# Performance work log

Measured on AMD Instinct MI355X. Metric: run time of the kernel, lower is better.

The kernel has to match this reference:

```python
import math
import jax, jax.numpy as jnp
import numpy as np

DIM = 4096
N_HEADS = 32
N_KV_HEADS = 8
HEAD_DIM = DIM // N_HEADS  # 128
N_REP = N_HEADS // N_KV_HEADS  # 4
BSZ = 2
SEQLEN = 2048
ROPE_THETA = 500000.0


def setup_inputs() -> dict:
    key = jax.random.key(0)
    ks = jax.random.split(key, 6)
    s = 0.02
    x = jax.random.normal(ks[0], (BSZ, SEQLEN, DIM), dtype=jnp.float32)
    wq = jax.random.normal(ks[1], (DIM, N_HEADS * HEAD_DIM), dtype=jnp.float32) * s
    wk = jax.random.normal(ks[2], (DIM, N_KV_HEADS * HEAD_DIM), dtype=jnp.float32) * s
    wv = jax.random.normal(ks[3], (DIM, N_KV_HEADS * HEAD_DIM), dtype=jnp.float32) * s
    wo = jax.random.normal(ks[4], (N_HEADS * HEAD_DIM, DIM), dtype=jnp.float32) * s
    # RoPE frequencies (real cos/sin form of complex freqs_cis)
    inv_freq = 1.0 / (ROPE_THETA ** (jnp.arange(0, HEAD_DIM, 2, dtype=jnp.float32) / HEAD_DIM))
    t = jnp.arange(SEQLEN, dtype=jnp.float32)
    angles = jnp.outer(t, inv_freq)  # [S, HEAD_DIM/2]
    freqs_cos = jnp.cos(angles)
    freqs_sin = jnp.sin(angles)
    # additive causal mask [S, S]: 0 on/below diag, -1e9 above
    mask = jnp.where(jnp.tril(jnp.ones((SEQLEN, SEQLEN), dtype=bool)), 0.0, -1e9).astype(jnp.float32)
    return {"x": x, "wq": wq, "wk": wk, "wv": wv, "wo": wo,
            "freqs_cos": freqs_cos, "freqs_sin": freqs_sin, "mask": mask,
            "start_pos": 0}


def _apply_rope(t, cos, sin):
    # t: [B, S, H, HD]; cos/sin: [S, HD/2] -> broadcast [1, S, 1, HD/2]
    b, s, h, hd = t.shape
    tr = t.reshape(b, s, h, hd // 2, 2)
    te, to = tr[..., 0], tr[..., 1]
    c = cos[None, :, None, :]
    sn = sin[None, :, None, :]
    oe = te * c - to * sn
    oo = te * sn + to * c
    return jnp.stack([oe, oo], axis=-1).reshape(b, s, h, hd)


def reference(x, wq, wk, wv, wo, freqs_cos, freqs_sin, mask, start_pos):
    bsz, seqlen, _ = x.shape
    xq = (x @ wq).reshape(bsz, seqlen, N_HEADS, HEAD_DIM)
    xk = (x @ wk).reshape(bsz, seqlen, N_KV_HEADS, HEAD_DIM)
    xv = (x @ wv).reshape(bsz, seqlen, N_KV_HEADS, HEAD_DIM)
    xq = _apply_rope(xq, freqs_cos, freqs_sin)
    xk = _apply_rope(xk, freqs_cos, freqs_sin)
    # prefill: cache[:start_pos+seqlen] == xk/xv (start_pos=0); GQA repeat
    keys = jnp.repeat(xk, N_REP, axis=2)    # [B, S, N_HEADS, HD]
    values = jnp.repeat(xv, N_REP, axis=2)
    q = xq.transpose(0, 2, 1, 3)            # [B, H, S, HD]
    k = keys.transpose(0, 2, 1, 3)
    v = values.transpose(0, 2, 1, 3)
    scores = jnp.einsum('bhqd,bhkd->bhqk', q, k) / math.sqrt(HEAD_DIM)
    scores = scores + mask[None, None, :, :]
    probs = jax.nn.softmax(scores.astype(jnp.float32), axis=-1).astype(q.dtype)
    ctx = jnp.einsum('bhqk,bhkd->bhqd', probs, v)
    out = ctx.transpose(0, 2, 1, 3).reshape(bsz, seqlen, N_HEADS * HEAD_DIM)
    return out @ wo
```

## Files before the change

### kernel.cpp

```cpp
#include <hip/hip_runtime.h>
#include <hip/hip_bf16.h>
#include <math.h>
#include <stdint.h>

#define DIM 4096
#define N_HEADS 32
#define N_KV_HEADS 8
#define HEAD_DIM 128
#define BSZ 2
#define SEQLEN 2048
#define BS (BSZ * SEQLEN)
#define KV_DIM (N_KV_HEADS * HEAD_DIM)

typedef unsigned short u16;
typedef __attribute__((ext_vector_type(8))) short bf16x8;
typedef __attribute__((ext_vector_type(4))) float f32x4;
typedef __attribute__((ext_vector_type(16))) float f32x16;
typedef __attribute__((ext_vector_type(8))) unsigned short u16x8;
typedef __attribute__((ext_vector_type(4))) unsigned short u16x4;

__device__ __forceinline__ u16 f2bf(float f) {
    __hip_bfloat16 h = __float2bfloat16(f);
    return *reinterpret_cast<u16*>(&h);
}
__device__ __forceinline__ float bf2f(u16 u) {
    __hip_bfloat16 h;
    *reinterpret_cast<u16*>(&h) = u;
    return __bfloat162float(h);
}
__device__ __forceinline__ uint32_t packbf(float a, float b) {
    return (uint32_t)f2bf(a) | ((uint32_t)f2bf(b) << 16);
}

#define GLOAD_LDS16(gptr, lptr)                                                      \
    __builtin_amdgcn_global_load_lds(                                                \
        reinterpret_cast<const __attribute__((address_space(1))) uint32_t*>(         \
            reinterpret_cast<uintptr_t>(gptr)),                                      \
        reinterpret_cast<__attribute__((address_space(3))) uint32_t*>(               \
            reinterpret_cast<uintptr_t>(lptr)),                                      \
        16, 0, 0)

__global__ void cvt_f32_bf16(const float* __restrict__ in, u16* __restrict__ out, int n4) {
    int i = blockIdx.x * blockDim.x + threadIdx.x;
    if (i >= n4) return;
    float4 v = reinterpret_cast<const float4*>(in)[i];
    u16x4 o;
    o.x = f2bf(v.x); o.y = f2bf(v.y); o.z = f2bf(v.z); o.w = f2bf(v.w);
    reinterpret_cast<u16x4*>(out)[i] = o;
}

__global__ __launch_bounds__(256) void transpose_f32_bf16(const float* __restrict__ in,
                                                          u16* __restrict__ out,
                                                          int K, int N) {
    __shared__ float tile[32][33];
    const int tx = threadIdx.x, ty = threadIdx.y;
    const int n0 = blockIdx.x * 32, k0 = blockIdx.y * 32;
#pragma unroll
    for (int i = 0; i < 4; ++i)
        tile[ty + 8 * i][tx] = in[(size_t)(k0 + ty + 8 * i) * N + n0 + tx];
    __syncthreads();
#pragma unroll
    for (int i = 0; i < 4; ++i)
        out[(size_t)(n0 + ty + 8 * i) * K + k0 + tx] = f2bf(tile[tx][ty + 8 * i]);
}

__global__ __launch_bounds__(256) void transpose_v_bf16(const u16* __restrict__ xv,
                                                        u16* __restrict__ xvT) {
    __shared__ u16 tile[32][33];
    const int tx = threadIdx.x, ty = threadIdx.y;
    const int k0 = blockIdx.x * 32, d0 = blockIdx.y * 32;
    const int bh = blockIdx.z;
    const int b = bh >> 3, hkv = bh & 7;
#pragma unroll
    for (int i = 0; i < 4; ++i)
        tile[ty + 8 * i][tx] =
            xv[((size_t)(b * SEQLEN) + k0 + ty + 8 * i) * KV_DIM + hkv * HEAD_DIM + d0 + tx];
    __syncthreads();
#pragma unroll
    for (int i = 0; i < 4; ++i)
        xvT[((size_t)bh * HEAD_DIM + d0 + ty + 8 * i) * SEQLEN + k0 + tx] = tile[tx][ty + 8 * i];
}

template <bool OUT_BF16>
__global__ __launch_bounds__(256) void gemm_mfma_bt(const u16* __restrict__ A,
                                                    const u16* __restrict__ BT,
                                                    void* __restrict__ Cv,
                                                    int M, int N, int K) {
    __shared__ __align__(16) u16 Al[128 * 64];
    __shared__ __align__(16) u16 Bl[128 * 64];

    const int tid  = threadIdx.x;
    const int wave = tid >> 6;
    const int lane = tid & 63;
    const int quad = lane >> 4;
    const int lm   = lane & 15;
    const size_t bm = (size_t)blockIdx.y * 128;
    const size_t bn = (size_t)blockIdx.x * 128;
    const int wm = (wave & 1) * 64;
    const int wn = (wave >> 1) * 64;

    const int slot = lane & 7;
    const int lrow = lane >> 3;
    const int csw  = slot ^ (lrow & 7);

    f32x4 acc[4][4] = {};

    for (int k0 = 0; k0 < K; k0 += 64) {
        __syncthreads();
#pragma unroll
        for (int i = 0; i < 4; ++i) {
            const int mloc = wave * 32 + i * 8 + lrow;
            const u16* gA = A  + (bm + mloc) * (size_t)K + k0 + csw * 8;
            const u16* gB = BT + (bn + mloc) * (size_t)K + k0 + csw * 8;
            u16* lA = &Al[(mloc * 8 + slot) * 8];
            u16* lB = &Bl[(mloc * 8 + slot) * 8];
            GLOAD_LDS16(gA, lA);
            GLOAD_LDS16(gB, lB);
        }
        __syncthreads();

#pragma unroll
        for (int ks8 = 0; ks8 < 8; ks8 += 4) {
            bf16x8 af[4], bfr[4];
            const int cc = ks8 + quad;
#pragma unroll
            for (int i = 0; i < 4; ++i) {
                const int m = wm + 16 * i + lm;
                af[i]  = *(const bf16x8*)&Al[(m * 8 + (cc ^ (m & 7))) * 8];
                const int n = wn + 16 * i + lm;
                bfr[i] = *(const bf16x8*)&Bl[(n * 8 + (cc ^ (n & 7))) * 8];
            }
#pragma unroll
            for (int i = 0; i < 4; ++i)
#pragma unroll
                for (int j = 0; j < 4; ++j)
                    acc[i][j] = __builtin_amdgcn_mfma_f32_16x16x32_bf16(af[i], bfr[j], acc[i][j], 0, 0, 0);
        }
    }

#pragma unroll
    for (int i = 0; i < 4; ++i) {
        const int mrow = wm + 16 * i + quad * 4;
#pragma unroll
        for (int j = 0; j < 4; ++j) {
            const int ncol = wn + 16 * j + lm;
#pragma unroll
            for (int r = 0; r < 4; ++r) {
                const size_t off = (bm + mrow + r) * (size_t)N + bn + ncol;
                const float v = acc[i][j][r];
                if constexpr (OUT_BF16) ((u16*)Cv)[off] = f2bf(v);
                else                    ((float*)Cv)[off] = v;
            }
        }
    }
}

__global__ void rope_kernel(u16* __restrict__ t,
                            const float* __restrict__ cosb,
                            const float* __restrict__ sinb,
                            int n_heads, int total_pairs) {
    int idx = blockIdx.x * blockDim.x + threadIdx.x;
    if (idx >= total_pairs) return;
    int p = idx & 63;
    int h = (idx >> 6) % n_heads;
    int bs = idx / (64 * n_heads);
    int s = bs & (SEQLEN - 1);

    float c = cosb[s * 64 + p];
    float sn = sinb[s * 64 + p];

    size_t base = (size_t)bs * (n_heads * HEAD_DIM) + h * HEAD_DIM + 2 * p;
    float e = bf2f(t[base]);
    float o = bf2f(t[base + 1]);
    t[base]     = f2bf(e * c - o * sn);
    t[base + 1] = f2bf(e * sn + o * c);
}

#define OPAD 132

__global__ __launch_bounds__(256, 2) void flash_attn_mfma(const u16* __restrict__ xq,
                                                          const u16* __restrict__ xk,
                                                          const u16* __restrict__ xvT,
                                                          u16* __restrict__ ctx) {
    __shared__ __align__(16) u16 LB[128 * OPAD];
    u16* Ks = LB;
    u16* Vt = LB + 64 * 16 * 8;

    const int qt  = (int)gridDim.x - 1 - (int)blockIdx.x;
    const int h   = blockIdx.y;
    const int b   = blockIdx.z;
    const int hkv = h >> 2;

    const int tid  = threadIdx.x;
    const int wave = tid >> 6;
    const int lane = tid & 63;
    const int hh   = lane >> 5;
    const int l31  = lane & 31;
    const int q0   = qt * 128;
    const int wq0  = q0 + wave * 32;
    const int qrow = wq0 + l31;
    const float C = 0.08838834764831845f * 1.44269504088896f;

    bf16x8 qf[8];
    {
        const u16* qp = xq + ((size_t)(b * SEQLEN) + qrow) * DIM + h * HEAD_DIM + hh * 8;
#pragma unroll
        for (int s = 0; s < 8; ++s) qf[s] = *(const bf16x8*)(qp + 16 * s);
    }

    const u16* xkb = xk + (size_t)(b * SEQLEN) * KV_DIM + hkv * HEAD_DIM;
    const u16* xvb = xvT + ((size_t)(b * N_KV_HEADS + hkv)) * HEAD_DIM * SEQLEN;

    float m_i = -INFINITY, l_i = 0.f;
    f32x16 acc[4] = {};

    const int nkt = 2 * qt + 2;
    for (int kt = 0; kt < nkt; ++kt) {
        const int k0 = kt * 64;
        __syncthreads();
#pragma unroll
        for (int i = 0; i < 4; ++i) {
            const int ci = i * 256 + tid;
            const int kr = ci >> 4, cp = ci & 15;
            GLOAD_LDS16(xkb + (size_t)(k0 + kr) * KV_DIM + (cp ^ (kr & 7)) * 8, &Ks[ci * 8]);
            const int dr = ci >> 3, cq = ci & 7;
            GLOAD_LDS16(xvb + (size_t)dr * SEQLEN + k0 + (cq ^ (dr & 7)) * 8, &Vt[ci * 8]);
        }
        __syncthreads();

        if (k0 > wq0 + 31) continue;

        f32x16 s[2] = {};
        __builtin_amdgcn_s_setprio(1);
#pragma unroll
        for (int step = 0; step < 8; ++step) {
#pragma unroll
            for (int ct = 0; ct < 2; ++ct) {
                const int krow = ct * 32 + l31;
                const int c = 2 * step + hh;
                bf16x8 kf = *(const bf16x8*)&Ks[(krow * 16 + (c ^ (krow & 7))) * 8];
                s[ct] = __builtin_amdgcn_mfma_f32_32x32x16_bf16(kf, qf[step], s[ct], 0, 0, 0);
            }
        }
        __builtin_amdgcn_s_setprio(0);

        if (k0 + 63 > wq0) {
#pragma unroll
            for (int ct = 0; ct < 2; ++ct)
#pragma unroll
                for (int r = 0; r < 16; ++r) {
                    const int kg = k0 + ct * 32 + (r & 3) + 8 * (r >> 2) + 4 * hh;
                    if (kg > qrow) s[ct][r] = -1e30f;
                }
        }

        float mx = s[0][0];
#pragma unroll
        for (int r = 1; r < 16; ++r) mx = fmaxf(mx, s[0][r]);
#pragma unroll
        for (int r = 0; r < 16; ++r) mx = fmaxf(mx, s[1][r]);
        mx = fmaxf(mx, __shfl_xor(mx, 32));
        const float nm = fmaxf(m_i, mx);
        const float alpha = exp2f((m_i - nm) * C);
        m_i = nm;
        float sum = 0.f;
#pragma unroll
        for (int ct = 0; ct < 2; ++ct)
#pragma unroll
            for (int r = 0; r < 16; ++r) {
                const float p = exp2f((s[ct][r] - nm) * C);
                s[ct][r] = p;
                sum += p;
            }
        sum += __shfl_xor(sum, 32);
        l_i = alpha * l_i + sum;

        bf16x8 pa[4];
#pragma unroll
        for (int ct = 0; ct < 2; ++ct)
#pragma unroll
            for (int kss = 0; kss < 2; ++kss) {
                const int base = 8 * kss;
                const uint32_t lo0 = packbf(s[ct][base + 0], s[ct][base + 1]);
                const uint32_t lo1 = packbf(s[ct][base + 2], s[ct][base + 3]);
                const uint32_t hi0 = packbf(s[ct][base + 4], s[ct][base + 5]);
                const uint32_t hi1 = packbf(s[ct][base + 6], s[ct][base + 7]);
                const uint32_t s0 = hh ? lo0 : hi0;
                const uint32_t s1 = hh ? lo1 : hi1;
                const uint32_t r0 = (uint32_t)__shfl_xor((int)s0, 32);
                const uint32_t r1 = (uint32_t)__shfl_xor((int)s1, 32);
                union { uint32_t u[4]; bf16x8 v; } pu;
                pu.u[0] = hh ? r0 : lo0;
                pu.u[1] = hh ? r1 : lo1;
                pu.u[2] = hh ? hi0 : r0;
                pu.u[3] = hh ? hi1 : r1;
                pa[2 * ct + kss] = pu.v;
            }

#pragma unroll
        for (int dt = 0; dt < 4; ++dt)
#pragma unroll
            for (int r = 0; r < 16; ++r) acc[dt][r] *= alpha;

        __builtin_amdgcn_s_setprio(1);
#pragma unroll
        for (int ks = 0; ks < 4; ++ks)
#pragma unroll
            for (int dt = 0; dt < 4; ++dt) {
                const int vrow = dt * 32 + l31;
                const int c = 2 * ks + hh;
                bf16x8 vf = *(const bf16x8*)&Vt[(vrow * 8 + (c ^ (vrow & 7))) * 8];
                acc[dt] = __builtin_amdgcn_mfma_f32_32x32x16_bf16(vf, pa[ks], acc[dt], 0, 0, 0);
            }
        __builtin_amdgcn_s_setprio(0);
    }

    __syncthreads();
    const float inv_l = 1.0f / l_i;
    const int q_l = wave * 32 + l31;
#pragma unroll
    for (int dt = 0; dt < 4; ++dt)
#pragma unroll
        for (int rp = 0; rp < 8; ++rp) {
            const int reg = 2 * rp;
            const int d = dt * 32 + (reg & 3) + 8 * (reg >> 2) + 4 * hh;
            *(uint32_t*)&LB[q_l * OPAD + d] =
                packbf(acc[dt][reg] * inv_l, acc[dt][reg + 1] * inv_l);
        }
    __syncthreads();
    {
        const int qr = tid >> 1, hf = tid & 1;
        u16* op = ctx + ((size_t)(b * SEQLEN) + q0 + qr) * DIM + h * HEAD_DIM + hf * 64;
        const u16* lp = &LB[qr * OPAD + hf * 64];
#pragma unroll
        for (int c = 0; c < 16; ++c)
            *(u16x4*)(op + 4 * c) = *(const u16x4*)(lp + 4 * c);
    }
}

extern "C" void kernel_launch(void* const* d_in, const int* in_sizes, int n_in,
                              void* d_out, int out_size, void* d_ws, size_t ws_size,
                              hipStream_t stream) {
    const float* x   = (const float*)d_in[0];
    const float* wq  = (const float*)d_in[1];
    const float* wk  = (const float*)d_in[2];
    const float* wv  = (const float*)d_in[3];
    const float* wo  = (const float*)d_in[4];
    const float* fc  = (const float*)d_in[5];
    const float* fs  = (const float*)d_in[6];
    float* out = (float*)d_out;

    u16* x_bf = (u16*)d_ws;
    u16* wqT  = x_bf + (size_t)BS * DIM;
    u16* wkT  = wqT + (size_t)DIM * DIM;
    u16* wvT  = wkT + (size_t)KV_DIM * DIM;
    u16* woT  = wvT + (size_t)KV_DIM * DIM;
    u16* xq   = woT + (size_t)DIM * DIM;
    u16* xk   = xq + (size_t)BS * DIM;
    u16* xv   = xk + (size_t)BS * KV_DIM;
    u16* ctx  = x_bf;
    u16* xvT  = wvT;

    {
        int n4 = BS * DIM / 4;
        cvt_f32_bf16<<<(n4 + 255) / 256, 256, 0, stream>>>(x, x_bf, n4);
        dim3 blk(32, 8);
        transpose_f32_bf16<<<dim3(DIM / 32, DIM / 32), blk, 0, stream>>>(wq, wqT, DIM, DIM);
        transpose_f32_bf16<<<dim3(KV_DIM / 32, DIM / 32), blk, 0, stream>>>(wk, wkT, DIM, KV_DIM);
        transpose_f32_bf16<<<dim3(KV_DIM / 32, DIM / 32), blk, 0, stream>>>(wv, wvT, DIM, KV_DIM);
        transpose_f32_bf16<<<dim3(DIM / 32, DIM / 32), blk, 0, stream>>>(wo, woT, DIM, DIM);
    }

    gemm_mfma_bt<true><<<dim3(DIM / 128, BS / 128), 256, 0, stream>>>(x_bf, wqT, xq, BS, DIM, DIM);
    gemm_mfma_bt<true><<<dim3(KV_DIM / 128, BS / 128), 256, 0, stream>>>(x_bf, wkT, xk, BS, KV_DIM, DIM);
    gemm_mfma_bt<true><<<dim3(KV_DIM / 128, BS / 128), 256, 0, stream>>>(x_bf, wvT, xv, BS, KV_DIM, DIM);

    transpose_v_bf16<<<dim3(SEQLEN / 32, HEAD_DIM / 32, BSZ * N_KV_HEADS), dim3(32, 8), 0, stream>>>(xv, xvT);

    {
        int total_q = BS * N_HEADS * 64;
        rope_kernel<<<(total_q + 255) / 256, 256, 0, stream>>>(xq, fc, fs, N_HEADS, total_q);
        int total_k = BS * N_KV_HEADS * 64;
        rope_kernel<<<(total_k + 255) / 256, 256, 0, stream>>>(xk, fc, fs, N_KV_HEADS, total_k);
    }

    flash_attn_mfma<<<dim3(SEQLEN / 128, N_HEADS, BSZ), 256, 0, stream>>>(xq, xk, xvT, ctx);

    gemm_mfma_bt<false><<<dim3(DIM / 128, BS / 128), 256, 0, stream>>>(ctx, woT, out, BS, DIM, DIM);
}
```

Baseline: 993.6 us.

## Share K/V tiles across two query heads per block and skip small rescales

Each attention block now uses 512 threads and handles two query heads that share one KV head. Every K/V tile loaded into LDS is reused by both heads, which halves K/V global traffic and the load work per head. It also adds a lazy online-softmax rescale: the running max and the accumulator are only updated when the new max exceeds the old by more than a threshold, which saves exponentials and multiplies. The risks are higher register pressure at 512 threads with launch bounds of 4, and a serialized two-pass epilogue for writing the outputs.

```diff
diff --git a/kernel.cpp b/kernel.cpp
--- a/kernel.cpp
+++ b/kernel.cpp
@@ -178,7 +178,7 @@
 
 #define OPAD 132
 
-__global__ __launch_bounds__(256, 2) void flash_attn_mfma(const u16* __restrict__ xq,
+__global__ __launch_bounds__(512, 4) void flash_attn_mfma(const u16* __restrict__ xq,
                                                           const u16* __restrict__ xk,
                                                           const u16* __restrict__ xvT,
                                                           u16* __restrict__ ctx) {
@@ -187,17 +187,18 @@
     u16* Vt = LB + 64 * 16 * 8;
 
     const int qt  = (int)gridDim.x - 1 - (int)blockIdx.x;
-    const int h   = blockIdx.y;
+    const int hp  = blockIdx.y;
     const int b   = blockIdx.z;
-    const int hkv = h >> 2;
+    const int hkv = hp >> 1;
 
     const int tid  = threadIdx.x;
     const int wave = tid >> 6;
     const int lane = tid & 63;
     const int hh   = lane >> 5;
     const int l31  = lane & 31;
+    const int h    = 2 * hp + (wave >> 2);
     const int q0   = qt * 128;
-    const int wq0  = q0 + wave * 32;
+    const int wq0  = q0 + (wave & 3) * 32;
     const int qrow = wq0 + l31;
     const float C = 0.08838834764831845f * 1.44269504088896f;
 
@@ -219,8 +220,8 @@
         const int k0 = kt * 64;
         __syncthreads();
 #pragma unroll
-        for (int i = 0; i < 4; ++i) {
-            const int ci = i * 256 + tid;
+        for (int i = 0; i < 2; ++i) {
+            const int ci = i * 512 + tid;
             const int kr = ci >> 4, cp = ci & 15;
             GLOAD_LDS16(xkb + (size_t)(k0 + kr) * KV_DIM + (cp ^ (kr & 7)) * 8, &Ks[ci * 8]);
             const int dr = ci >> 3, cq = ci & 7;
@@ -260,15 +261,20 @@
 #pragma unroll
         for (int r = 0; r < 16; ++r) mx = fmaxf(mx, s[1][r]);
         mx = fmaxf(mx, __shfl_xor(mx, 32));
-        const float nm = fmaxf(m_i, mx);
-        const float alpha = exp2f((m_i - nm) * C);
-        m_i = nm;
+
+        const bool keep = __all((mx - m_i) * C <= 8.0f);
+        float alpha = 1.0f;
+        if (!keep) {
+            const float nm = fmaxf(m_i, mx);
+            alpha = exp2f((m_i - nm) * C);
+            m_i = nm;
+        }
         float sum = 0.f;
 #pragma unroll
         for (int ct = 0; ct < 2; ++ct)
 #pragma unroll
             for (int r = 0; r < 16; ++r) {
-                const float p = exp2f((s[ct][r] - nm) * C);
+                const float p = exp2f((s[ct][r] - m_i) * C);
                 s[ct][r] = p;
                 sum += p;
             }
@@ -297,10 +303,12 @@
                 pa[2 * ct + kss] = pu.v;
             }
 
-#pragma unroll
-        for (int dt = 0; dt < 4; ++dt)
-#pragma unroll
-            for (int r = 0; r < 16; ++r) acc[dt][r] *= alpha;
+        if (!keep) {
+#pragma unroll
+            for (int dt = 0; dt < 4; ++dt)
+#pragma unroll
+                for (int r = 0; r < 16; ++r) acc[dt][r] *= alpha;
+        }
 
         __builtin_amdgcn_s_setprio(1);
 #pragma unroll
@@ -317,24 +325,31 @@
 
     __syncthreads();
     const float inv_l = 1.0f / l_i;
-    const int q_l = wave * 32 + l31;
-#pragma unroll
-    for (int dt = 0; dt < 4; ++dt)
-#pragma unroll
-        for (int rp = 0; rp < 8; ++rp) {
-            const int reg = 2 * rp;
-            const int d = dt * 32 + (reg & 3) + 8 * (reg >> 2) + 4 * hh;
-            *(uint32_t*)&LB[q_l * OPAD + d] =
-                packbf(acc[dt][reg] * inv_l, acc[dt][reg + 1] * inv_l);
-        }
-    __syncthreads();
-    {
-        const int qr = tid >> 1, hf = tid & 1;
-        u16* op = ctx + ((size_t)(b * SEQLEN) + q0 + qr) * DIM + h * HEAD_DIM + hf * 64;
-        const u16* lp = &LB[qr * OPAD + hf * 64];
-#pragma unroll
-        for (int c = 0; c < 16; ++c)
-            *(u16x4*)(op + 4 * c) = *(const u16x4*)(lp + 4 * c);
+#pragma unroll
+    for (int g = 0; g < 2; ++g) {
+        if ((wave >> 2) == g) {
+            const int q_l = (wave & 3) * 32 + l31;
+#pragma unroll
+            for (int dt = 0; dt < 4; ++dt)
+#pragma unroll
+                for (int rp = 0; rp < 8; ++rp) {
+                    const int reg = 2 * rp;
+                    const int d = dt * 32 + (reg & 3) + 8 * (reg >> 2) + 4 * hh;
+                    *(uint32_t*)&LB[q_l * OPAD + d] =
+                        packbf(acc[dt][reg] * inv_l, acc[dt][reg + 1] * inv_l);
+                }
+        }
+        __syncthreads();
+        {
+            const int qr = tid >> 2, seg = tid & 3;
+            u16* op = ctx + ((size_t)(b * SEQLEN) + q0 + qr) * DIM
+                      + (2 * hp + g) * HEAD_DIM + seg * 32;
+            const u16* lp = &LB[qr * OPAD + seg * 32];
+#pragma unroll
+            for (int c2 = 0; c2 < 8; ++c2)
+                *(u16x4*)(op + 4 * c2) = *(const u16x4*)(lp + 4 * c2);
+        }
+        __syncthreads();
     }
 }
 
@@ -384,7 +399,7 @@
         rope_kernel<<<(total_k + 255) / 256, 256, 0, stream>>>(xk, fc, fs, N_KV_HEADS, total_k);
     }
 
-    flash_attn_mfma<<<dim3(SEQLEN / 128, N_HEADS, BSZ), 256, 0, stream>>>(xq, xk, xvT, ctx);
+    flash_attn_mfma<<<dim3(SEQLEN / 128, N_HEADS / 2, BSZ), 512, 0, stream>>>(xq, xk, xvT, ctx);
 
     gemm_mfma_bt<false><<<dim3(DIM / 128, BS / 128), 256, 0, stream>>>(ctx, woT, out, BS, DIM, DIM);
 }
```

After: 1.140 ms. 14.8% more time.
